# Kernel tuning notes

Hardware: AMD Instinct MI355X
Metric: run time of the kernel (lower is better)

The kernel has to match this reference:

```python
import jax, jax.numpy as jnp
import numpy as np

B, P, E = 16, 1024, 768
HID, HEADS = 768, 12
DH = HID // HEADS  # 64
EPS = 1e-5


def setup_inputs() -> dict:
    key = jax.random.key(0)
    ks = jax.random.split(key, 4)
    return {
        "x": jax.random.normal(ks[0], (B, P, E), dtype=jnp.float32),
        "ln_weight": jnp.ones((P, E), dtype=jnp.float32),
        "ln_bias": jnp.zeros((P, E), dtype=jnp.float32),
        "qkv": jax.random.normal(ks[1], (E, 3 * HID), dtype=jnp.float32),
        "lin_w": jax.random.normal(ks[2], (HID, E), dtype=jnp.float32) * 0.02,
        "lin_b": jax.random.normal(ks[3], (E,), dtype=jnp.float32) * 0.02,
    }


def reference(x, ln_weight, ln_bias, qkv, lin_w, lin_b):
    # LayerNorm over the last TWO dims (patches, emb), per torch nn.LayerNorm((P, E))
    mean = jnp.mean(x, axis=(-2, -1), keepdims=True)
    var = jnp.var(x, axis=(-2, -1), keepdims=True)
    xn = (x - mean) / jnp.sqrt(var + EPS) * ln_weight + ln_bias

    # QKV projection: [B,P,E] @ [E,3*HID] -> [B,P,3*HID]
    proj = xn @ qkv
    # view(B,P,heads,-1) then permute -> [B,heads,P,3*DH]; chunk along last dim
    proj = proj.reshape(B, P, HEADS, 3 * DH).transpose(0, 2, 1, 3)
    q, k, v = proj[..., :DH], proj[..., DH:2 * DH], proj[..., 2 * DH:]

    # Softmax-free attention: (Q K^T) V
    atten = jnp.einsum("bhqd,bhkd->bhqk", q, k)  # [B,H,P,P]
    out = jnp.einsum("bhqk,bhkd->bhqd", atten, v)  # [B,H,P,DH]

    out = out.transpose(0, 2, 1, 3).reshape(B, P, HID)
    # dropout p=0.0 (eval) -> identity
    out = jax.nn.relu(out @ lin_w + lin_b)
    return out + x
```

## Files before the change

### kernel.cpp

```cpp
#include <hip/hip_runtime.h>
#include <hip/hip_bf16.h>
#include <cstdint>

#define BB   16
#define PP   1024
#define EE   768
#define HID  768
#define NH   12
#define DH   64
#define NPB  (PP * EE)
#define MROWS (BB * PP)

typedef __bf16 bf16_t;
typedef __bf16 bf16x8 __attribute__((ext_vector_type(8)));
typedef float  f32x4  __attribute__((ext_vector_type(4)));

__device__ __forceinline__ void gld16(const void* g, void* l) {
    __builtin_amdgcn_global_load_lds(
        (const __attribute__((address_space(1))) void*)(uintptr_t)g,
        (__attribute__((address_space(3))) void*)(uint32_t)(uintptr_t)l,
        16, 0, 0);
}

__global__ __launch_bounds__(256) void stats1_kernel(const float* __restrict__ x,
                                                     float* __restrict__ part) {
    int bid = blockIdx.x;
    int b = bid >> 6, s = bid & 63;
    const float4* xp = (const float4*)(x + (size_t)b * NPB + (size_t)s * 12288);
    float sum = 0.f, ss = 0.f;
#pragma unroll
    for (int i = 0; i < 12; ++i) {
        float4 v = xp[i * 256 + threadIdx.x];
        sum += v.x + v.y + v.z + v.w;
        ss  += v.x * v.x + v.y * v.y + v.z * v.z + v.w * v.w;
    }
#pragma unroll
    for (int off = 32; off > 0; off >>= 1) {
        sum += __shfl_down(sum, off, 64);
        ss  += __shfl_down(ss,  off, 64);
    }
    __shared__ float tmp[8];
    int wave = threadIdx.x >> 6, lane = threadIdx.x & 63;
    if (lane == 0) { tmp[wave * 2] = sum; tmp[wave * 2 + 1] = ss; }
    __syncthreads();
    if (threadIdx.x == 0) {
        part[bid * 2]     = tmp[0] + tmp[2] + tmp[4] + tmp[6];
        part[bid * 2 + 1] = tmp[1] + tmp[3] + tmp[5] + tmp[7];
    }
}

__global__ __launch_bounds__(256) void prep_kernel(const float* __restrict__ qkvw,
                                                   const float* __restrict__ linw,
                                                   const float* __restrict__ part,
                                                   bf16_t* __restrict__ qkvT,
                                                   bf16_t* __restrict__ lwT,
                                                   float* __restrict__ stats) {
    int bid = blockIdx.x;
    if (bid < 576) {
        __shared__ float lds[64][65];
        const float* src; bf16_t* dst; int r0, c0, W;
        if (bid < 432) {
            int tr = bid / 36, tc = bid - tr * 36;
            r0 = tr * 64; c0 = tc * 64; src = qkvw; W = 2304; dst = qkvT;
        } else {
            int bb = bid - 432;
            int tr = bb / 12, tc = bb - tr * 12;
            r0 = tr * 64; c0 = tc * 64; src = linw; W = 768; dst = lwT;
        }
        int t = threadIdx.x;
        int rr = t >> 4, cc4 = (t & 15) * 4;
#pragma unroll
        for (int j = 0; j < 4; ++j) {
            float4 v = *(const float4*)(src + (size_t)(r0 + rr + j * 16) * W + c0 + cc4);
            lds[rr + j * 16][cc4 + 0] = v.x;
            lds[rr + j * 16][cc4 + 1] = v.y;
            lds[rr + j * 16][cc4 + 2] = v.z;
            lds[rr + j * 16][cc4 + 3] = v.w;
        }
        __syncthreads();
        int cl = t >> 3, rgl = (t & 7) * 8;
#pragma unroll
        for (int jj = 0; jj < 2; ++jj) {
            int c = jj * 32 + cl;
            union { bf16_t h[8]; uint4 u; } o;
#pragma unroll
            for (int k = 0; k < 8; ++k) o.h[k] = (bf16_t)lds[rgl + k][c];
            *(uint4*)(dst + (size_t)(c0 + c) * 768 + r0 + rgl) = o.u;
        }
    } else {
        int wave = threadIdx.x >> 6, lane = threadIdx.x & 63;
#pragma unroll
        for (int j = 0; j < 4; ++j) {
            int b = wave * 4 + j;
            float sum = part[(b * 64 + lane) * 2];
            float ss  = part[(b * 64 + lane) * 2 + 1];
#pragma unroll
            for (int off = 32; off > 0; off >>= 1) {
                sum += __shfl_down(sum, off, 64);
                ss  += __shfl_down(ss,  off, 64);
            }
            if (lane == 0) {
                const float inv_n = 1.f / (float)NPB;
                float mean = sum * inv_n;
                float var  = ss * inv_n - mean * mean;
                stats[b * 2]     = mean;
                stats[b * 2 + 1] = rsqrtf(var + 1e-5f);
            }
        }
    }
}

__global__ __launch_bounds__(256) void ln_apply_kernel(const float* __restrict__ x,
                                                       const float* __restrict__ lnw,
                                                       const float* __restrict__ lnb,
                                                       const float* __restrict__ stats,
                                                       bf16_t* __restrict__ xn) {
    int i = (blockIdx.x * 256 + threadIdx.x) * 8;
    int b = i / NPB;
    int r = i - b * NPB;
    float mean = stats[b * 2], rstd = stats[b * 2 + 1];
    float4 x0 = *(const float4*)(x + i),     x1 = *(const float4*)(x + i + 4);
    float4 w0 = *(const float4*)(lnw + r),   w1 = *(const float4*)(lnw + r + 4);
    float4 c0 = *(const float4*)(lnb + r),   c1 = *(const float4*)(lnb + r + 4);
    union { bf16_t h[8]; uint4 u; } o;
    o.h[0] = (bf16_t)((x0.x - mean) * rstd * w0.x + c0.x);
    o.h[1] = (bf16_t)((x0.y - mean) * rstd * w0.y + c0.y);
    o.h[2] = (bf16_t)((x0.z - mean) * rstd * w0.z + c0.z);
    o.h[3] = (bf16_t)((x0.w - mean) * rstd * w0.w + c0.w);
    o.h[4] = (bf16_t)((x1.x - mean) * rstd * w1.x + c1.x);
    o.h[5] = (bf16_t)((x1.y - mean) * rstd * w1.y + c1.y);
    o.h[6] = (bf16_t)((x1.z - mean) * rstd * w1.z + c1.z);
    o.h[7] = (bf16_t)((x1.w - mean) * rstd * w1.w + c1.w);
    *(uint4*)(xn + i) = o.u;
}

__device__ __forceinline__ void core256_bk32(const bf16_t* __restrict__ A,
                                             const bf16_t* __restrict__ Bt,
                                             int mBase, int nBase,
                                             f32x4 acc[8][4], bf16_t* smem) {
    const int t = threadIdx.x, lane = t & 63, wave = t >> 6;
    const int wm = wave >> 2, wn = wave & 3;
    const int m16 = lane & 15, quad = lane >> 4;

    const bf16_t* gsrc[4];
    int ldst[4];
#pragma unroll
    for (int j = 0; j < 2; ++j) {
        int c = t + 512 * j;
        int l = c >> 3, lg = ((c & 7) - (l & 7)) & 7;
        int row = l + (lg >> 2) * 128, kc = lg & 3;
        gsrc[j]     = A  + (size_t)(mBase + row) * 768 + kc * 8;
        ldst[j]     = c * 8;
        gsrc[2 + j] = Bt + (size_t)(nBase + row) * 768 + kc * 8;
        ldst[2 + j] = 8192 + c * 8;
    }

    int aOff[8], bOff[4];
#pragma unroll
    for (int mf = 0; mf < 8; ++mf) {
        int l = mf * 16 + m16;
        aOff[mf] = l * 64 + (((wm * 4 + quad) + (l & 7)) & 7) * 8;
    }
#pragma unroll
    for (int nf = 0; nf < 4; ++nf) {
        int l = (wn & 1) * 64 + nf * 16 + m16;
        bOff[nf] = 8192 + l * 64 + ((((wn >> 1) * 4 + quad) + (l & 7)) & 7) * 8;
    }

    const f32x4 z = {0.f, 0.f, 0.f, 0.f};
#pragma unroll
    for (int mf = 0; mf < 8; ++mf)
#pragma unroll
        for (int nf = 0; nf < 4; ++nf) acc[mf][nf] = z;

#pragma unroll
    for (int j = 0; j < 4; ++j) gld16(gsrc[j], smem + ldst[j]);
#pragma unroll
    for (int j = 0; j < 4; ++j) gld16(gsrc[j] + 32, smem + 16384 + ldst[j]);

#pragma unroll
    for (int step = 0; step < 24; ++step) {
        const int cur = (step % 3) * 16384;
        asm volatile("s_waitcnt lgkmcnt(0)" ::: "memory");
        __builtin_amdgcn_sched_barrier(0);
        __builtin_amdgcn_s_barrier();
        if (step + 2 < 24) {
            const int nb = ((step + 2) % 3) * 16384;
            const int kq = (step + 2) * 32;
#pragma unroll
            for (int j = 0; j < 4; ++j)
                gld16(gsrc[j] + kq, smem + nb + ldst[j]);
        }
        if (step < 22)       asm volatile("s_waitcnt vmcnt(8)" ::: "memory");
        else if (step == 22) asm volatile("s_waitcnt vmcnt(4)" ::: "memory");
        else                 asm volatile("s_waitcnt vmcnt(0)" ::: "memory");
        __builtin_amdgcn_sched_barrier(0);
        __builtin_amdgcn_s_barrier();

        bf16x8 af0[4], bfv[4], af1[4];
#pragma unroll
        for (int f = 0; f < 4; ++f) af0[f] = *(const bf16x8*)(smem + cur + aOff[f]);
#pragma unroll
        for (int f = 0; f < 4; ++f) bfv[f] = *(const bf16x8*)(smem + cur + bOff[f]);
#pragma unroll
        for (int f = 0; f < 4; ++f) af1[f] = *(const bf16x8*)(smem + cur + aOff[4 + f]);
        __builtin_amdgcn_s_setprio(1);
#pragma unroll
        for (int mf = 0; mf < 4; ++mf)
#pragma unroll
            for (int nf = 0; nf < 4; ++nf)
                acc[mf][nf] = __builtin_amdgcn_mfma_f32_16x16x32_bf16(
                    af0[mf], bfv[nf], acc[mf][nf], 0, 0, 0);
#pragma unroll
        for (int mf = 0; mf < 4; ++mf)
#pragma unroll
            for (int nf = 0; nf < 4; ++nf)
                acc[4 + mf][nf] = __builtin_amdgcn_mfma_f32_16x16x32_bf16(
                    af1[mf], bfv[nf], acc[4 + mf][nf], 0, 0, 0);
        __builtin_amdgcn_s_setprio(0);
    }
}

__global__ __launch_bounds__(512, 2) void gemm_qkv_kernel(const bf16_t* __restrict__ xn,
                                                          const bf16_t* __restrict__ qkvT,
                                                          bf16_t* __restrict__ q,
                                                          bf16_t* __restrict__ kt,
                                                          bf16_t* __restrict__ vt) {
    __shared__ bf16_t smem[49152];
    const int t = threadIdx.x, lane = t & 63, wave = t >> 6;
    const int wm = wave >> 2, wn = wave & 3;
    const int m16 = lane & 15, quad = lane >> 4;

    const int lb = blockIdx.y * 9 + blockIdx.x;
    const int id = (lb & 7) * 72 + (lb >> 3);
    const int tx = id % 9, ty = id / 9;
    const int mBase = ty * 256, nBase = tx * 256;

    f32x4 acc[8][4];
    core256_bk32(xn, qkvT, mBase, nBase, acc, smem);

    __syncthreads();
    bf16_t* slot = smem + wave * 4608;
    const int b = mBase >> 10, p0 = mBase & 1023;
    const int g64 = tx * 4 + wn;
    const int cls = g64 % 3, h = g64 / 3;

#pragma unroll
    for (int pass = 0; pass < 2; ++pass) {
        if (cls == 0) {
#pragma unroll
            for (int mf = 0; mf < 4; ++mf)
#pragma unroll
                for (int nf = 0; nf < 4; ++nf)
#pragma unroll
                    for (int i = 0; i < 4; ++i)
                        slot[(mf * 16 + quad * 4 + i) * 72 + nf * 16 + m16] =
                            (bf16_t)acc[pass * 4 + mf][nf][i];
            asm volatile("s_waitcnt lgkmcnt(0)" ::: "memory");
            __builtin_amdgcn_sched_barrier(0);
#pragma unroll
            for (int j = 0; j < 8; ++j) {
                int r = j * 8 + (lane >> 3), cc = lane & 7;
                bf16x8 val = *(const bf16x8*)(slot + r * 72 + cc * 8);
                *(bf16x8*)(q + ((size_t)(b * 1024 + p0 + wm * 128 + pass * 64 + r)) * 768 +
                           h * 64 + cc * 8) = val;
            }
        } else {
            bf16_t* dst = (cls == 1) ? kt : vt;
            const size_t bh = (size_t)(b * 12 + h);
#pragma unroll
            for (int mf = 0; mf < 4; ++mf)
#pragma unroll
                for (int nf = 0; nf < 4; ++nf) {
                    int c = nf * 16 + m16;
                    union { bf16_t hh[4]; uint2 u; } pk;
#pragma unroll
                    for (int i = 0; i < 4; ++i)
                        pk.hh[i] = (bf16_t)acc[pass * 4 + mf][nf][i];
                    *(uint2*)(slot + c * 72 + mf * 16 + quad * 4) = pk.u;
                }
            asm volatile("s_waitcnt lgkmcnt(0)" ::: "memory");
            __builtin_amdgcn_sched_barrier(0);
#pragma unroll
            for (int j = 0; j < 8; ++j) {
                int c = (lane >> 3) + j * 8, r8 = (lane & 7) * 8;
                bf16x8 val = *(const bf16x8*)(slot + c * 72 + r8);
                *(bf16x8*)(dst + (bh * 64 + c) * 1024 + p0 + wm * 128 +
                           pass * 64 + r8) = val;
            }
        }
        if (pass == 0) {
            asm volatile("s_waitcnt lgkmcnt(0)" ::: "memory");
            __builtin_amdgcn_sched_barrier(0);
        }
    }
}

__global__ __launch_bounds__(256) void kvu_kernel(const bf16_t* __restrict__ kt,
                                                  const bf16_t* __restrict__ vt,
                                                  const bf16_t* __restrict__ lwT,
                                                  bf16_t* __restrict__ ut) {
    __shared__ float red[4 * 64 * 65];
    const int bh = blockIdx.x;
    const int b = bh / NH, h = bh - b * NH;
    const bf16_t* Kb = kt + (size_t)bh * DH * PP;
    const bf16_t* Vb = vt + (size_t)bh * DH * PP;
    const int t = threadIdx.x;
    const int lane = t & 63, wave = t >> 6;
    const int m16 = lane & 15, quad = lane >> 4;
    const f32x4 z = {0.f, 0.f, 0.f, 0.f};

    {
        f32x4 acc[4][4];
#pragma unroll
        for (int mm = 0; mm < 4; ++mm)
#pragma unroll
            for (int nn = 0; nn < 4; ++nn) acc[mm][nn] = z;
        for (int ks = 0; ks < 8; ++ks) {
            int kb = wave * 256 + ks * 32 + quad * 8;
            bf16x8 af[4], bfv[4];
#pragma unroll
            for (int mm = 0; mm < 4; ++mm)
                af[mm] = *(const bf16x8*)(Kb + (size_t)(mm * 16 + m16) * PP + kb);
#pragma unroll
            for (int nn = 0; nn < 4; ++nn)
                bfv[nn] = *(const bf16x8*)(Vb + (size_t)(nn * 16 + m16) * PP + kb);
#pragma unroll
            for (int mm = 0; mm < 4; ++mm)
#pragma unroll
                for (int nn = 0; nn < 4; ++nn)
                    acc[mm][nn] = __builtin_amdgcn_mfma_f32_16x16x32_bf16(
                        af[mm], bfv[nn], acc[mm][nn], 0, 0, 0);
        }
#pragma unroll
        for (int mm = 0; mm < 4; ++mm)
#pragma unroll
            for (int nn = 0; nn < 4; ++nn)
#pragma unroll
                for (int i = 0; i < 4; ++i)
                    red[wave * 4160 + (mm * 16 + quad * 4 + i) * 65 + nn * 16 + m16] =
                        acc[mm][nn][i];
    }
    __syncthreads();

    const int wm = wave >> 1, wn = wave & 1;
    bf16x8 ah[2][2], al[2][2];
#pragma unroll
    for (int mm = 0; mm < 2; ++mm)
#pragma unroll
        for (int ks = 0; ks < 2; ++ks) {
            int d1 = wm * 32 + mm * 16 + m16;
            int base = d1 * 65 + ks * 32 + quad * 8;
#pragma unroll
            for (int e = 0; e < 8; ++e) {
                float s = red[base + e] + red[4160 + base + e] +
                          red[8320 + base + e] + red[12480 + base + e];
                bf16_t hi = (bf16_t)s;
                ah[mm][ks][e] = hi;
                al[mm][ks][e] = (bf16_t)(s - (float)hi);
            }
        }

#pragma unroll
    for (int ny = 0; ny < 3; ++ny) {
        const int nBase = ny * 256;
        f32x4 acc2[2][8];
#pragma unroll
        for (int mm = 0; mm < 2; ++mm)
#pragma unroll
            for (int nn = 0; nn < 8; ++nn) acc2[mm][nn] = z;
#pragma unroll
        for (int ks = 0; ks < 2; ++ks) {
            bf16x8 bfr[8];
#pragma unroll
            for (int nn = 0; nn < 8; ++nn)
                bfr[nn] = *(const bf16x8*)(
                    lwT + (size_t)(nBase + wn * 128 + nn * 16 + m16) * 768 +
                    h * 64 + ks * 32 + quad * 8);
#pragma unroll
            for (int mm = 0; mm < 2; ++mm)
#pragma unroll
                for (int nn = 0; nn < 8; ++nn) {
                    acc2[mm][nn] = __builtin_amdgcn_mfma_f32_16x16x32_bf16(
                        ah[mm][ks], bfr[nn], acc2[mm][nn], 0, 0, 0);
                    acc2[mm][nn] = __builtin_amdgcn_mfma_f32_16x16x32_bf16(
                        al[mm][ks], bfr[nn], acc2[mm][nn], 0, 0, 0);
                }
        }
#pragma unroll
        for (int mm = 0; mm < 2; ++mm)
#pragma unroll
            for (int nn = 0; nn < 8; ++nn) {
                int e  = nBase + wn * 128 + nn * 16 + m16;
                int d1 = wm * 32 + mm * 16 + quad * 4;
                union { bf16_t hh[4]; uint2 u; } pk;
#pragma unroll
                for (int i = 0; i < 4; ++i) pk.hh[i] = (bf16_t)acc2[mm][nn][i];
                *(uint2*)(ut + ((size_t)b * 768 + e) * 768 + h * 64 + d1) = pk.u;
            }
    }
}

__global__ __launch_bounds__(512, 2) void gemm_out_kernel(const bf16_t* __restrict__ q,
                                                          const bf16_t* __restrict__ ut,
                                                          const float* __restrict__ linb,
                                                          const float* __restrict__ x,
                                                          float* __restrict__ out) {
    __shared__ bf16_t smem[49152];
    const int lb = blockIdx.y * 3 + blockIdx.x;
    const int id = (lb & 7) * 24 + (lb >> 3);
    const int tx = id % 3, ty = id / 3;
    const int mBase = ty * 256, nBase = tx * 256;
    const int b = mBase >> 10;

    f32x4 acc[8][4];
    core256_bk32(q, ut + (size_t)b * 768 * 768, mBase, nBase, acc, smem);

    const int lane = threadIdx.x & 63, wave = threadIdx.x >> 6;
    const int wm = wave >> 2, wn = wave & 3;
    const int m16 = lane & 15, quad = lane >> 4;
#pragma unroll
    for (int mf = 0; mf < 8; ++mf) {
#pragma unroll
        for (int i = 0; i < 4; ++i) {
            size_t row = mBase + wm * 128 + mf * 16 + quad * 4 + i;
#pragma unroll
            for (int nf = 0; nf < 4; ++nf) {
                int col = nBase + wn * 64 + nf * 16 + m16;
                float v = acc[mf][nf][i] + linb[col];
                v = fmaxf(v, 0.f) + x[row * EE + col];
                out[row * EE + col] = v;
            }
        }
    }
}

extern "C" void kernel_launch(void* const* d_in, const int* in_sizes, int n_in,
                              void* d_out, int out_size, void* d_ws, size_t ws_size,
                              hipStream_t stream) {
    const float* x    = (const float*)d_in[0];
    const float* lnw  = (const float*)d_in[1];
    const float* lnb  = (const float*)d_in[2];
    const float* qkvw = (const float*)d_in[3];
    const float* linw = (const float*)d_in[4];
    const float* linb = (const float*)d_in[5];
    float* out = (float*)d_out;
    char* ws = (char*)d_ws;

    float*  part  = (float*)(ws + 0);
    float*  stats = (float*)(ws + 8192);
    bf16_t* xn    = (bf16_t*)(ws + 8448);
    bf16_t* qkvT  = (bf16_t*)(ws + 25174272);
    bf16_t* lwT   = (bf16_t*)(ws + 28713216);
    bf16_t* q     = (bf16_t*)(ws + 29892864);
    bf16_t* kt    = (bf16_t*)(ws + 55058688);
    bf16_t* vt    = (bf16_t*)(ws + 80224512);
    bf16_t* ut    = xn;

    stats1_kernel<<<dim3(BB * 64), dim3(256), 0, stream>>>(x, part);
    prep_kernel<<<dim3(577), dim3(256), 0, stream>>>(qkvw, linw, part, qkvT, lwT, stats);
    ln_apply_kernel<<<dim3(6144), dim3(256), 0, stream>>>(x, lnw, lnb, stats, xn);
    gemm_qkv_kernel<<<dim3(9, 64), dim3(512), 0, stream>>>(xn, qkvT, q, kt, vt);
    kvu_kernel<<<dim3(192), dim3(256), 0, stream>>>(kt, vt, lwT, ut);
    gemm_out_kernel<<<dim3(3, 64), dim3(512), 0, stream>>>(q, ut, linb, x, out);
}
```

Measured before the change: 257.7 us.

## Split GEMM k-step into two phases with interleaved loads and new LDS swizzle

Rewrites the shared 256x256 GEMM core used by the QKV and output GEMMs. Each k-step now runs in two half-phases, each issuing half of the next tile's global-to-LDS loads between its own LDS reads and MFMAs. The LDS layout moves from an 8-chunk XOR-style swizzle over 64-element rows to a 4-chunk rotation over 32-element rows, with matching changes to the load and fragment offsets. The goal is to spread memory traffic across the MFMA work, at the cost of more barriers per step and a riskier ordering of waitcnt against barriers.

```diff
diff --git a/kernel.cpp b/kernel.cpp
--- a/kernel.cpp
+++ b/kernel.cpp
@@ -134,37 +134,35 @@
     *(uint4*)(xn + i) = o.u;
 }
 
-__device__ __forceinline__ void core256_bk32(const bf16_t* __restrict__ A,
-                                             const bf16_t* __restrict__ Bt,
-                                             int mBase, int nBase,
-                                             f32x4 acc[8][4], bf16_t* smem) {
+__device__ __forceinline__ void core256_ph(const bf16_t* __restrict__ A,
+                                           const bf16_t* __restrict__ Bt,
+                                           int mBase, int nBase,
+                                           f32x4 acc[8][4], bf16_t* smem) {
     const int t = threadIdx.x, lane = t & 63, wave = t >> 6;
     const int wm = wave >> 2, wn = wave & 3;
     const int m16 = lane & 15, quad = lane >> 4;
 
-    const bf16_t* gsrc[4];
-    int ldst[4];
+    const bf16_t* ga[2]; const bf16_t* gb[2]; int la[2], lb[2];
 #pragma unroll
     for (int j = 0; j < 2; ++j) {
         int c = t + 512 * j;
-        int l = c >> 3, lg = ((c & 7) - (l & 7)) & 7;
-        int row = l + (lg >> 2) * 128, kc = lg & 3;
-        gsrc[j]     = A  + (size_t)(mBase + row) * 768 + kc * 8;
-        ldst[j]     = c * 8;
-        gsrc[2 + j] = Bt + (size_t)(nBase + row) * 768 + kc * 8;
-        ldst[2 + j] = 8192 + c * 8;
+        int l = c >> 2, lg = ((c & 3) - (l & 3)) & 3;
+        ga[j] = A  + (size_t)(mBase + l) * 768 + lg * 8;
+        la[j] = c * 8;
+        gb[j] = Bt + (size_t)(nBase + l) * 768 + lg * 8;
+        lb[j] = 8192 + c * 8;
     }
 
     int aOff[8], bOff[4];
 #pragma unroll
     for (int mf = 0; mf < 8; ++mf) {
-        int l = mf * 16 + m16;
-        aOff[mf] = l * 64 + (((wm * 4 + quad) + (l & 7)) & 7) * 8;
+        int l = wm * 128 + mf * 16 + m16;
+        aOff[mf] = l * 32 + ((quad + l) & 3) * 8;
     }
 #pragma unroll
     for (int nf = 0; nf < 4; ++nf) {
-        int l = (wn & 1) * 64 + nf * 16 + m16;
-        bOff[nf] = 8192 + l * 64 + ((((wn >> 1) * 4 + quad) + (l & 7)) & 7) * 8;
+        int l = wn * 64 + nf * 16 + m16;
+        bOff[nf] = 8192 + l * 32 + ((quad + l) & 3) * 8;
     }
 
     const f32x4 z = {0.f, 0.f, 0.f, 0.f};
@@ -174,50 +172,58 @@
         for (int nf = 0; nf < 4; ++nf) acc[mf][nf] = z;
 
 #pragma unroll
-    for (int j = 0; j < 4; ++j) gld16(gsrc[j], smem + ldst[j]);
-#pragma unroll
-    for (int j = 0; j < 4; ++j) gld16(gsrc[j] + 32, smem + 16384 + ldst[j]);
-
-#pragma unroll
-    for (int step = 0; step < 24; ++step) {
-        const int cur = (step % 3) * 16384;
+    for (int j = 0; j < 2; ++j) { gld16(ga[j], smem + la[j]); gld16(gb[j], smem + lb[j]); }
+#pragma unroll
+    for (int j = 0; j < 2; ++j) { gld16(ga[j] + 32, smem + 16384 + la[j]); gld16(gb[j] + 32, smem + 16384 + lb[j]); }
+    asm volatile("s_waitcnt vmcnt(4)" ::: "memory");
+    __builtin_amdgcn_sched_barrier(0);
+    __builtin_amdgcn_s_barrier();
+
+#pragma unroll
+    for (int kt = 0; kt < 24; ++kt) {
+        const int cur = (kt % 3) * 16384;
+        const int nxt = ((kt + 2) % 3) * 16384;
+        const int kq  = (kt + 2) * 32;
+        bf16x8 af[4], bfv[4];
+
+#pragma unroll
+        for (int f = 0; f < 4; ++f) af[f]  = *(const bf16x8*)(smem + cur + aOff[f]);
+#pragma unroll
+        for (int f = 0; f < 4; ++f) bfv[f] = *(const bf16x8*)(smem + cur + bOff[f]);
+        if (kt + 2 < 24) { gld16(ga[0] + kq, smem + nxt + la[0]); gld16(gb[0] + kq, smem + nxt + lb[0]); }
+        __builtin_amdgcn_s_barrier();
         asm volatile("s_waitcnt lgkmcnt(0)" ::: "memory");
         __builtin_amdgcn_sched_barrier(0);
-        __builtin_amdgcn_s_barrier();
-        if (step + 2 < 24) {
-            const int nb = ((step + 2) % 3) * 16384;
-            const int kq = (step + 2) * 32;
-#pragma unroll
-            for (int j = 0; j < 4; ++j)
-                gld16(gsrc[j] + kq, smem + nb + ldst[j]);
-        }
-        if (step < 22)       asm volatile("s_waitcnt vmcnt(8)" ::: "memory");
-        else if (step == 22) asm volatile("s_waitcnt vmcnt(4)" ::: "memory");
-        else                 asm volatile("s_waitcnt vmcnt(0)" ::: "memory");
-        __builtin_amdgcn_sched_barrier(0);
-        __builtin_amdgcn_s_barrier();
-
-        bf16x8 af0[4], bfv[4], af1[4];
-#pragma unroll
-        for (int f = 0; f < 4; ++f) af0[f] = *(const bf16x8*)(smem + cur + aOff[f]);
-#pragma unroll
-        for (int f = 0; f < 4; ++f) bfv[f] = *(const bf16x8*)(smem + cur + bOff[f]);
-#pragma unroll
-        for (int f = 0; f < 4; ++f) af1[f] = *(const bf16x8*)(smem + cur + aOff[4 + f]);
         __builtin_amdgcn_s_setprio(1);
 #pragma unroll
         for (int mf = 0; mf < 4; ++mf)
 #pragma unroll
             for (int nf = 0; nf < 4; ++nf)
                 acc[mf][nf] = __builtin_amdgcn_mfma_f32_16x16x32_bf16(
-                    af0[mf], bfv[nf], acc[mf][nf], 0, 0, 0);
+                    af[mf], bfv[nf], acc[mf][nf], 0, 0, 0);
+        __builtin_amdgcn_s_setprio(0);
+        __builtin_amdgcn_s_barrier();
+
+#pragma unroll
+        for (int f = 0; f < 4; ++f) af[f] = *(const bf16x8*)(smem + cur + aOff[4 + f]);
+        if (kt + 2 < 24) { gld16(ga[1] + kq, smem + nxt + la[1]); gld16(gb[1] + kq, smem + nxt + lb[1]); }
+        __builtin_amdgcn_s_barrier();
+        asm volatile("s_waitcnt lgkmcnt(0)" ::: "memory");
+        __builtin_amdgcn_sched_barrier(0);
+        __builtin_amdgcn_s_setprio(1);
 #pragma unroll
         for (int mf = 0; mf < 4; ++mf)
 #pragma unroll
             for (int nf = 0; nf < 4; ++nf)
                 acc[4 + mf][nf] = __builtin_amdgcn_mfma_f32_16x16x32_bf16(
-                    af1[mf], bfv[nf], acc[4 + mf][nf], 0, 0, 0);
+                    af[mf], bfv[nf], acc[4 + mf][nf], 0, 0, 0);
         __builtin_amdgcn_s_setprio(0);
+        if (kt < 23) {
+            if (kt < 22) asm volatile("s_waitcnt vmcnt(4)" ::: "memory");
+            else         asm volatile("s_waitcnt vmcnt(0)" ::: "memory");
+            __builtin_amdgcn_sched_barrier(0);
+        }
+        __builtin_amdgcn_s_barrier();
     }
 }
 
@@ -237,7 +243,7 @@
     const int mBase = ty * 256, nBase = tx * 256;
 
     f32x4 acc[8][4];
-    core256_bk32(xn, qkvT, mBase, nBase, acc, smem);
+    core256_ph(xn, qkvT, mBase, nBase, acc, smem);
 
     __syncthreads();
     bf16_t* slot = smem + wave * 4608;
@@ -414,7 +420,7 @@
     const int b = mBase >> 10;
 
     f32x4 acc[8][4];
-    core256_bk32(q, ut + (size_t)b * 768 * 768, mBase, nBase, acc, smem);
+    core256_ph(q, ut + (size_t)b * 768 * 768, mBase, nBase, acc, smem);
 
     const int lane = threadIdx.x & 63, wave = threadIdx.x >> 6;
     const int wm = wave >> 2, wn = wave & 3;
```

Result: no change. 254.1 us (-1.4%).
